# Optimization experiments

Measured on AMD Instinct MI355X. Metric: run time of the kernel, lower is better.

The kernel has to match this reference:

```python
import jax, jax.numpy as jnp
import numpy as np

K = 7  # kernel_size

def setup_inputs() -> dict:
    key = jax.random.key(0)
    k1, k2, k3 = jax.random.split(key, 3)
    X = jax.random.normal(k1, (32, 256, 64, 64), dtype=jnp.float32)
    # PyTorch Conv2d default init: uniform(-b, b), b = 1/sqrt(fan_in), fan_in = 2*7*7
    bound = 1.0 / np.sqrt(2 * K * K)
    conv_w = jax.random.uniform(k2, (1, 2, K, K), dtype=jnp.float32, minval=-bound, maxval=bound)
    conv_b = jax.random.uniform(k3, (1,), dtype=jnp.float32, minval=-bound, maxval=bound)
    return {"X": X, "conv_w": conv_w, "conv_b": conv_b}

def reference(X, conv_w, conv_b):
    # channel-wise max and mean pooling -> [B, 2, H, W]
    max_pool = jnp.max(X, axis=1, keepdims=True)
    avg_pool = jnp.mean(X, axis=1, keepdims=True)
    pool_out = jnp.concatenate([max_pool, avg_pool], axis=1)
    # 2 -> 1 channel 7x7 conv, stride 1, padding 3 (SAME for odd K)
    out = jax.lax.conv_general_dilated(
        pool_out, conv_w,
        window_strides=(1, 1),
        padding=[(K // 2, K // 2), (K // 2, K // 2)],
        dimension_numbers=("NCHW", "OIHW", "NCHW"),
    ) + conv_b[None, :, None, None]
    gate = jax.nn.sigmoid(out)  # [B, 1, H, W]
    return gate * X
```

## Files before the change

### kernel.cpp

```cpp
#include <hip/hip_runtime.h>
#include <math.h>

#define Bn 32
#define Cn 256
#define Hn 64
#define Wn 64
#define HWn (Hn * Wn)
#define CHWn (Cn * HWn)

typedef float f32x4 __attribute__((ext_vector_type(4)));

__global__ __launch_bounds__(256) void pool_kernel(const float* __restrict__ X,
                                                   float* __restrict__ maxp,
                                                   float* __restrict__ avgp) {
    const int tid   = threadIdx.x;
    const int w4    = tid & 15;
    const int c_sub = tid >> 4;
    const int b     = blockIdx.x >> 6;
    const int h     = blockIdx.x & 63;

    const f32x4* Xb = (const f32x4*)(X + (size_t)b * CHWn + (size_t)h * Wn) + w4;

    f32x4 mx = { -INFINITY, -INFINITY, -INFINITY, -INFINITY };
    f32x4 sm = { 0.f, 0.f, 0.f, 0.f };
    #pragma unroll
    for (int k = 0; k < 16; ++k) {
        const int c = c_sub * 16 + k;
        f32x4 v = Xb[(size_t)c * (HWn / 4)];
        mx.x = fmaxf(mx.x, v.x); mx.y = fmaxf(mx.y, v.y);
        mx.z = fmaxf(mx.z, v.z); mx.w = fmaxf(mx.w, v.w);
        sm += v;
    }

    __shared__ f32x4 smax[256];
    __shared__ f32x4 ssum[256];
    smax[tid] = mx;
    ssum[tid] = sm;
    __syncthreads();

    #pragma unroll
    for (int s = 128; s >= 16; s >>= 1) {
        if (tid < s) {
            f32x4 a = smax[tid], c = smax[tid + s];
            a.x = fmaxf(a.x, c.x); a.y = fmaxf(a.y, c.y);
            a.z = fmaxf(a.z, c.z); a.w = fmaxf(a.w, c.w);
            smax[tid] = a;
            ssum[tid] += ssum[tid + s];
        }
        __syncthreads();
    }

    if (tid < 16) {
        f32x4 m = smax[tid];
        f32x4 a = ssum[tid] * (1.0f / (float)Cn);
        const int o = b * (HWn / 4) + h * 16 + tid;
        ((f32x4*)maxp)[o] = m;
        ((f32x4*)avgp)[o] = a;
    }
}

__global__ __launch_bounds__(256) void conv_scale_kernel(const float* __restrict__ X,
                                                         const float* __restrict__ maxp,
                                                         const float* __restrict__ avgp,
                                                         const float* __restrict__ wgt,
                                                         const float* __restrict__ bias,
                                                         float* __restrict__ out) {
    __shared__ float ws[98];
    __shared__ float part[4][64];
    __shared__ float gate[64];

    const int tid = threadIdx.x;
    const int b = blockIdx.x >> 6;
    const int h = blockIdx.x & 63;

    if (tid < 98) ws[tid] = wgt[tid];
    __syncthreads();

    {
        const int x = tid & 63;
        const int g = tid >> 6;
        const float* mp = maxp + b * HWn;
        const float* ap = avgp + b * HWn;
        float acc = 0.f;
        #pragma unroll
        for (int ii = 0; ii < 2; ++ii) {
            const int i = g + ii * 4;
            if (i > 6) continue;
            const int yy = h + i - 3;
            if (yy < 0 || yy >= Hn) continue;
            #pragma unroll
            for (int j = 0; j < 7; ++j) {
                const int xx = x + j - 3;
                if (xx < 0 || xx >= Wn) continue;
                const int o = yy * Wn + xx;
                acc += ws[i * 7 + j] * mp[o] + ws[49 + i * 7 + j] * ap[o];
            }
        }
        part[g][x] = acc;
    }
    __syncthreads();

    if (tid < 64) {
        const float acc = bias[0] + part[0][tid] + part[1][tid] + part[2][tid] + part[3][tid];
        gate[tid] = 1.0f / (1.0f + expf(-acc));
    }
    __syncthreads();

    const int w4 = tid & 15;
    const int c0 = tid >> 4;
    const f32x4 g = ((const f32x4*)gate)[w4];

    const f32x4* X4 = (const f32x4*)(X   + (size_t)b * CHWn + (size_t)h * Wn) + w4;
    f32x4*       O4 = (f32x4*)      (out + (size_t)b * CHWn + (size_t)h * Wn) + w4;

    #pragma unroll
    for (int k = 0; k < 16; ++k) {
        const int c = k * 16 + c0;
        const size_t off = (size_t)c * (HWn / 4);
        f32x4 v = X4[off];
        v *= g;
        __builtin_nontemporal_store(v, O4 + off);
    }
}

extern "C" void kernel_launch(void* const* d_in, const int* in_sizes, int n_in,
                              void* d_out, int out_size, void* d_ws, size_t ws_size,
                              hipStream_t stream) {
    const float* X      = (const float*)d_in[0];
    const float* conv_w = (const float*)d_in[1];
    const float* conv_b = (const float*)d_in[2];
    float* out = (float*)d_out;

    float* maxp = (float*)d_ws;
    float* avgp = maxp + Bn * HWn;

    pool_kernel<<<Bn * Hn, 256, 0, stream>>>(X, maxp, avgp);

    conv_scale_kernel<<<Bn * Hn, 256, 0, stream>>>(X, maxp, avgp, conv_w, conv_b, out);
}
```

Baseline: 68.18 us.

## Fuse pool and conv-scale into one persistent kernel with grid barrier

Merges the pooling and conv/gate/scale kernels into a single launch of 1024 blocks, each handling two rows. A global atomic barrier in workspace separates the pooling phase from the conv phase. The second pass walks channels in reverse so the most recently read data is more likely still in L2/MALL. The goal is to remove a kernel launch gap and gain cache reuse of X between the two passes. In exchange it needs all 1024 blocks co-resident to avoid deadlock and adds a memset and a spin wait.

```diff
diff --git a/kernel.cpp b/kernel.cpp
--- a/kernel.cpp
+++ b/kernel.cpp
@@ -7,119 +7,132 @@
 #define Wn 64
 #define HWn (Hn * Wn)
 #define CHWn (Cn * HWn)
+#define NBLK 1024
+#define RPB 2
 
 typedef float f32x4 __attribute__((ext_vector_type(4)));
 
-__global__ __launch_bounds__(256) void pool_kernel(const float* __restrict__ X,
-                                                   float* __restrict__ maxp,
-                                                   float* __restrict__ avgp) {
-    const int tid   = threadIdx.x;
-    const int w4    = tid & 15;
-    const int c_sub = tid >> 4;
-    const int b     = blockIdx.x >> 6;
-    const int h     = blockIdx.x & 63;
-
-    const f32x4* Xb = (const f32x4*)(X + (size_t)b * CHWn + (size_t)h * Wn) + w4;
-
-    f32x4 mx = { -INFINITY, -INFINITY, -INFINITY, -INFINITY };
-    f32x4 sm = { 0.f, 0.f, 0.f, 0.f };
-    #pragma unroll
-    for (int k = 0; k < 16; ++k) {
-        const int c = c_sub * 16 + k;
-        f32x4 v = Xb[(size_t)c * (HWn / 4)];
-        mx.x = fmaxf(mx.x, v.x); mx.y = fmaxf(mx.y, v.y);
-        mx.z = fmaxf(mx.z, v.z); mx.w = fmaxf(mx.w, v.w);
-        sm += v;
-    }
+__global__ __launch_bounds__(256, 4) void fused_all(const float* __restrict__ X,
+                                                    const float* __restrict__ wgt,
+                                                    const float* __restrict__ bias,
+                                                    float* __restrict__ out,
+                                                    float* __restrict__ maxp,
+                                                    float* __restrict__ avgp,
+                                                    unsigned* __restrict__ bar) {
+    const int tid = threadIdx.x;
+    const int w4  = tid & 15;
+    const int c0  = tid >> 4;
 
     __shared__ f32x4 smax[256];
     __shared__ f32x4 ssum[256];
-    smax[tid] = mx;
-    ssum[tid] = sm;
-    __syncthreads();
-
-    #pragma unroll
-    for (int s = 128; s >= 16; s >>= 1) {
-        if (tid < s) {
-            f32x4 a = smax[tid], c = smax[tid + s];
-            a.x = fmaxf(a.x, c.x); a.y = fmaxf(a.y, c.y);
-            a.z = fmaxf(a.z, c.z); a.w = fmaxf(a.w, c.w);
-            smax[tid] = a;
-            ssum[tid] += ssum[tid + s];
-        }
-        __syncthreads();
-    }
-
-    if (tid < 16) {
-        f32x4 m = smax[tid];
-        f32x4 a = ssum[tid] * (1.0f / (float)Cn);
-        const int o = b * (HWn / 4) + h * 16 + tid;
-        ((f32x4*)maxp)[o] = m;
-        ((f32x4*)avgp)[o] = a;
-    }
-}
-
-__global__ __launch_bounds__(256) void conv_scale_kernel(const float* __restrict__ X,
-                                                         const float* __restrict__ maxp,
-                                                         const float* __restrict__ avgp,
-                                                         const float* __restrict__ wgt,
-                                                         const float* __restrict__ bias,
-                                                         float* __restrict__ out) {
     __shared__ float ws[98];
     __shared__ float part[4][64];
     __shared__ float gate[64];
 
-    const int tid = threadIdx.x;
-    const int b = blockIdx.x >> 6;
-    const int h = blockIdx.x & 63;
+    if (tid < 98) ws[tid] = wgt[tid];
 
-    if (tid < 98) ws[tid] = wgt[tid];
+    const int gr0 = blockIdx.x * RPB;
+
+    #pragma unroll
+    for (int rr = 0; rr < RPB; ++rr) {
+        const int gr = gr0 + rr;
+        const int b = gr >> 6;
+        const int h = gr & 63;
+        const f32x4* Xb = (const f32x4*)(X + (size_t)b * CHWn + (size_t)h * Wn) + w4;
+
+        f32x4 mx = { -INFINITY, -INFINITY, -INFINITY, -INFINITY };
+        f32x4 sm = { 0.f, 0.f, 0.f, 0.f };
+        #pragma unroll
+        for (int kk = 0; kk < 16; ++kk) {
+            const int c = kk * 16 + c0;
+            f32x4 v = Xb[(size_t)c * (HWn / 4)];
+            mx.x = fmaxf(mx.x, v.x); mx.y = fmaxf(mx.y, v.y);
+            mx.z = fmaxf(mx.z, v.z); mx.w = fmaxf(mx.w, v.w);
+            sm += v;
+        }
+
+        if (rr) __syncthreads();
+        smax[tid] = mx;
+        ssum[tid] = sm;
+        __syncthreads();
+
+        #pragma unroll
+        for (int s = 128; s >= 16; s >>= 1) {
+            if (tid < s) {
+                f32x4 a = smax[tid], c = smax[tid + s];
+                a.x = fmaxf(a.x, c.x); a.y = fmaxf(a.y, c.y);
+                a.z = fmaxf(a.z, c.z); a.w = fmaxf(a.w, c.w);
+                smax[tid] = a;
+                ssum[tid] += ssum[tid + s];
+            }
+            __syncthreads();
+        }
+
+        if (tid < 16) {
+            const int o = gr * 16 + tid;
+            ((f32x4*)maxp)[o] = smax[tid];
+            ((f32x4*)avgp)[o] = ssum[tid] * (1.0f / (float)Cn);
+        }
+    }
+
     __syncthreads();
-
-    {
-        const int x = tid & 63;
-        const int g = tid >> 6;
-        const float* mp = maxp + b * HWn;
-        const float* ap = avgp + b * HWn;
-        float acc = 0.f;
-        #pragma unroll
-        for (int ii = 0; ii < 2; ++ii) {
-            const int i = g + ii * 4;
-            if (i > 6) continue;
-            const int yy = h + i - 3;
-            if (yy < 0 || yy >= Hn) continue;
-            #pragma unroll
-            for (int j = 0; j < 7; ++j) {
-                const int xx = x + j - 3;
-                if (xx < 0 || xx >= Wn) continue;
-                const int o = yy * Wn + xx;
-                acc += ws[i * 7 + j] * mp[o] + ws[49 + i * 7 + j] * ap[o];
-            }
-        }
-        part[g][x] = acc;
+    if (tid == 0) {
+        __threadfence();
+        __hip_atomic_fetch_add(bar, 1u, __ATOMIC_ACQ_REL, __HIP_MEMORY_SCOPE_AGENT);
+        while (__hip_atomic_load(bar, __ATOMIC_ACQUIRE, __HIP_MEMORY_SCOPE_AGENT) < NBLK)
+            __builtin_amdgcn_s_sleep(2);
     }
     __syncthreads();
-
-    if (tid < 64) {
-        const float acc = bias[0] + part[0][tid] + part[1][tid] + part[2][tid] + part[3][tid];
-        gate[tid] = 1.0f / (1.0f + expf(-acc));
-    }
-    __syncthreads();
-
-    const int w4 = tid & 15;
-    const int c0 = tid >> 4;
-    const f32x4 g = ((const f32x4*)gate)[w4];
-
-    const f32x4* X4 = (const f32x4*)(X   + (size_t)b * CHWn + (size_t)h * Wn) + w4;
-    f32x4*       O4 = (f32x4*)      (out + (size_t)b * CHWn + (size_t)h * Wn) + w4;
+    __threadfence();
 
     #pragma unroll
-    for (int k = 0; k < 16; ++k) {
-        const int c = k * 16 + c0;
-        const size_t off = (size_t)c * (HWn / 4);
-        f32x4 v = X4[off];
-        v *= g;
-        __builtin_nontemporal_store(v, O4 + off);
+    for (int rr = 0; rr < RPB; ++rr) {
+        const int gr = gr0 + rr;
+        const int b = gr >> 6;
+        const int h = gr & 63;
+
+        {
+            const int x = tid & 63;
+            const int g = tid >> 6;
+            const float* mp = maxp + b * HWn;
+            const float* ap = avgp + b * HWn;
+            float acc = 0.f;
+            #pragma unroll
+            for (int ii = 0; ii < 2; ++ii) {
+                const int i = g + ii * 4;
+                if (i > 6) continue;
+                const int yy = h + i - 3;
+                if (yy < 0 || yy >= Hn) continue;
+                #pragma unroll
+                for (int j = 0; j < 7; ++j) {
+                    const int xx = x + j - 3;
+                    if (xx < 0 || xx >= Wn) continue;
+                    const int o = yy * Wn + xx;
+                    acc += ws[i * 7 + j] * mp[o] + ws[49 + i * 7 + j] * ap[o];
+                }
+            }
+            part[g][x] = acc;
+        }
+        __syncthreads();
+
+        if (tid < 64) {
+            const float acc = bias[0] + part[0][tid] + part[1][tid] + part[2][tid] + part[3][tid];
+            gate[tid] = 1.0f / (1.0f + expf(-acc));
+        }
+        __syncthreads();
+
+        const f32x4 g4 = ((const f32x4*)gate)[w4];
+        const f32x4* X4 = (const f32x4*)(X   + (size_t)b * CHWn + (size_t)h * Wn) + w4;
+        f32x4*       O4 = (f32x4*)      (out + (size_t)b * CHWn + (size_t)h * Wn) + w4;
+
+        #pragma unroll
+        for (int k = 15; k >= 0; --k) {
+            const int c = k * 16 + c0;
+            const size_t off = (size_t)c * (HWn / 4);
+            f32x4 v = X4[off];
+            v *= g4;
+            __builtin_nontemporal_store(v, O4 + off);
+        }
     }
 }
 
@@ -133,8 +146,8 @@
 
     float* maxp = (float*)d_ws;
     float* avgp = maxp + Bn * HWn;
+    unsigned* bar = (unsigned*)((char*)d_ws + (1u << 20));
 
-    pool_kernel<<<Bn * Hn, 256, 0, stream>>>(X, maxp, avgp);
-
-    conv_scale_kernel<<<Bn * Hn, 256, 0, stream>>>(X, maxp, avgp, conv_w, conv_b, out);
+    hipMemsetAsync(bar, 0, sizeof(unsigned), stream);
+    fused_all<<<NBLK, 256, 0, stream>>>(X, conv_w, conv_b, out, maxp, avgp, bar);
 }
```

Measured after the change: 262.2 us. 285% more time.
